# Kernel tuning notes

Measured on AMD Instinct MI355X. Metric: run time of the kernel, lower is better.

The kernel has to match this reference:

```python
import jax, jax.numpy as jnp
import numpy as np

N_NODES = 100000
N_FEAT = 128
HIDDEN = 64
OUT = 16
N_EDGES = 3200000
N_POS = 500000
N_NEG = 500000


def setup_inputs() -> dict:
    key = jax.random.key(0)
    ks = jax.random.split(key, 8)
    x = jax.random.normal(ks[0], (N_NODES, N_FEAT), dtype=jnp.float32)
    edge_index = jax.random.randint(ks[1], (2, N_EDGES), 0, N_NODES, dtype=jnp.int64)
    pos_edge_index = jax.random.randint(ks[2], (2, N_POS), 0, N_NODES, dtype=jnp.int64)
    neg_edge_index = jax.random.randint(ks[3], (2, N_NEG), 0, N_NODES, dtype=jnp.int64)
    W1 = jax.random.normal(ks[4], (N_FEAT, HIDDEN), dtype=jnp.float32) * (1.0 / np.sqrt(N_FEAT))
    b1 = jnp.zeros((HIDDEN,), dtype=jnp.float32)
    W2 = jax.random.normal(ks[5], (HIDDEN, OUT), dtype=jnp.float32) * (1.0 / np.sqrt(HIDDEN))
    b2 = jnp.zeros((OUT,), dtype=jnp.float32)
    return {"x": x, "edge_index": edge_index, "pos_edge_index": pos_edge_index,
            "neg_edge_index": neg_edge_index, "W1": W1, "b1": b1, "W2": W2, "b2": b2}


def gcn_conv(x, W, b, src, dst):
    """PyG GCNConv with add_self_loops=True: D^-1/2 (A+I) D^-1/2 X W + b."""
    n = x.shape[0]
    h = x @ W  # [N, out]
    # degree including self-loop (+1)
    deg = jax.ops.segment_sum(jnp.ones(dst.shape, dtype=h.dtype), dst, num_segments=n) + 1.0
    dis = jax.lax.rsqrt(deg)  # deg >= 1, never inf
    coef = dis[src] * dis[dst]  # [E]
    agg = jax.ops.segment_sum(h[src] * coef[:, None], dst, num_segments=n)
    # self-loop message: norm = dis[i]*dis[i]
    agg = agg + h * (dis * dis)[:, None]
    return agg + b


def reference(x, edge_index, pos_edge_index, neg_edge_index, W1, b1, W2, b2):
    src, dst = edge_index[0], edge_index[1]
    z = jax.nn.relu(gcn_conv(x, W1, b1, src, dst))
    z = gcn_conv(z, W2, b2, src, dst)  # [N, 16]
    ei = jnp.concatenate([pos_edge_index, neg_edge_index], axis=-1)  # [2, P+Q]
    logits = jnp.sum(z[ei[0]] * z[ei[1]], axis=-1)  # [P+Q]
    return logits
```

## Files before the change

kernel.cpp:

```cpp
#include <hip/hip_runtime.h>

#define F 128
#define H 64
#define O 16

#define BSHIFT 7
#define BSZ 128
#define NSUB 8
#define SUBCAP 768
#define ACHUNK 8192
#define XS 136

typedef _Float16 half8_t __attribute__((ext_vector_type(8)));
typedef _Float16 half4_t __attribute__((ext_vector_type(4)));
typedef float f32x4 __attribute__((ext_vector_type(4)));

__global__ void k_bcur2(int* __restrict__ bcur, int NC) {
    int i = blockIdx.x * blockDim.x + threadIdx.x;
    if (i < NC) bcur[i] = i * SUBCAP;
}

__global__ __launch_bounds__(512) void k_bucketA(const int* __restrict__ src,
                                                 const int* __restrict__ dstv,
                                                 int* __restrict__ bcur,
                                                 int* __restrict__ bdata, int E) {
    __shared__ int hist[1024];
    for (int t = threadIdx.x; t < 1024; t += 512) hist[t] = 0;
    __syncthreads();
    int base = blockIdx.x * ACHUNK;
    int end = min(base + ACHUNK, E);
    for (int i = base + threadIdx.x; i < end; i += 512) {
        atomicAdd(&hist[dstv[i] >> BSHIFT], 1);
    }
    __syncthreads();
    int sub = blockIdx.x & (NSUB - 1);
    for (int b = threadIdx.x; b < 1024; b += 512) {
        int c = hist[b];
        if (c > 0) hist[b] = atomicAdd(&bcur[b * NSUB + sub], c);
    }
    __syncthreads();
    for (int i = base + threadIdx.x; i < end; i += 512) {
        int d = dstv[i];
        int b = d >> BSHIFT;
        int pos = atomicAdd(&hist[b], 1);
        bdata[pos] = (src[i] << BSHIFT) | (d & (BSZ - 1));
    }
}

__global__ __launch_bounds__(256) void k_bdeg(const int* __restrict__ bdata,
                                              const int* __restrict__ bcur,
                                              int* __restrict__ deg, int N) {
    __shared__ int h[BSZ];
    int b = blockIdx.x;
    int node0 = b << BSHIFT;
    int nloc = min(BSZ, N - node0);
    for (int t = threadIdx.x; t < BSZ; t += 256) h[t] = 0;
    __syncthreads();
    for (int s = 0; s < NSUB; s++) {
        int start = (b * NSUB + s) * SUBCAP;
        int end = bcur[b * NSUB + s];
        for (int p = start + threadIdx.x; p < end; p += 256)
            atomicAdd(&h[bdata[p] & (BSZ - 1)], 1);
    }
    __syncthreads();
    for (int t = threadIdx.x; t < nloc; t += 256) deg[node0 + t] = h[t];
}

__global__ void k_dis(const int* __restrict__ deg, float* __restrict__ dis, int N) {
    int i = blockIdx.x * blockDim.x + threadIdx.x;
    if (i < N) dis[i] = rsqrtf((float)deg[i] + 1.0f);
}

__global__ void k_scan1(const int* __restrict__ deg, int* __restrict__ local,
                        int* __restrict__ partials, int N) {
    __shared__ int s[256];
    int tid = threadIdx.x;
    int i = blockIdx.x * 256 + tid;
    int v = (i < N) ? deg[i] : 0;
    s[tid] = v;
    __syncthreads();
    for (int off = 1; off < 256; off <<= 1) {
        int t = (tid >= off) ? s[tid - off] : 0;
        __syncthreads();
        s[tid] += t;
        __syncthreads();
    }
    if (i < N) local[i] = s[tid] - v;
    if (tid == 255) partials[blockIdx.x] = s[255];
}

__global__ void k_scan2(int* __restrict__ partials, int NB) {
    __shared__ int s[1024];
    int tid = threadIdx.x;
    int v = (tid < NB) ? partials[tid] : 0;
    s[tid] = v;
    __syncthreads();
    for (int off = 1; off < 1024; off <<= 1) {
        int t = (tid >= off) ? s[tid - off] : 0;
        __syncthreads();
        s[tid] += t;
        __syncthreads();
    }
    partials[tid] = s[tid] - v;
}

__global__ void k_scan3(int* __restrict__ row_ptr, const int* __restrict__ partials,
                        int N, int E) {
    int i = blockIdx.x * blockDim.x + threadIdx.x;
    if (i < N) {
        row_ptr[i] += partials[i >> 8];
    } else if (i == N) {
        row_ptr[N] = E;
    }
}

__global__ __launch_bounds__(256) void k_bplace(const int* __restrict__ bdata,
                                                const int* __restrict__ bcur,
                                                const int* __restrict__ row_ptr,
                                                int* __restrict__ col, int N) {
    __shared__ int cur[BSZ];
    int b = blockIdx.x;
    int node0 = b << BSHIFT;
    int nloc = min(BSZ, N - node0);
    for (int t = threadIdx.x; t < nloc; t += 256) cur[t] = row_ptr[node0 + t];
    __syncthreads();
    for (int s = 0; s < NSUB; s++) {
        int start = (b * NSUB + s) * SUBCAP;
        int end = bcur[b * NSUB + s];
        for (int p = start + threadIdx.x; p < end; p += 256) {
            int v = bdata[p];
            int pos = atomicAdd(&cur[v & (BSZ - 1)], 1);
            col[pos] = v >> BSHIFT;
        }
    }
}

__global__ void k_wprep(const float* __restrict__ W1, _Float16* __restrict__ wt_hi,
                        _Float16* __restrict__ wt_lo) {
    int idx = blockIdx.x * 256 + threadIdx.x;
    int c = idx >> 7, k = idx & 127;
    float w = W1[k * H + c];
    _Float16 hi = (_Float16)w;
    wt_hi[idx] = hi;
    wt_lo[idx] = (_Float16)(w - (float)hi);
}

__global__ __launch_bounds__(256) void k_gemm1(const float* __restrict__ x,
                                               const _Float16* __restrict__ wt_hi,
                                               const _Float16* __restrict__ wt_lo,
                                               const float* __restrict__ dis,
                                               _Float16* __restrict__ h1p, int N) {
    __shared__ _Float16 xh[64 * XS], xl[64 * XS], wh[64 * XS], wl[64 * XS];
    int tid = threadIdx.x;
    int row0 = blockIdx.x * 64;
#pragma unroll
    for (int i = 0; i < 8; i++) {
        int idx = i * 256 + tid;
        int r = idx >> 5;
        int c = (idx & 31) * 4;
        int rr = row0 + r; if (rr >= N) rr = N - 1;
        float4 v = *(const float4*)(x + (size_t)rr * F + c);
        half4_t h = {(_Float16)v.x, (_Float16)v.y, (_Float16)v.z, (_Float16)v.w};
        half4_t l = {(_Float16)(v.x - (float)h[0]), (_Float16)(v.y - (float)h[1]),
                     (_Float16)(v.z - (float)h[2]), (_Float16)(v.w - (float)h[3])};
        *(half4_t*)(xh + r * XS + c) = h;
        *(half4_t*)(xl + r * XS + c) = l;
    }
#pragma unroll
    for (int i = 0; i < 4; i++) {
        int idx = i * 256 + tid;
        int c = idx >> 4;
        int k8 = (idx & 15) * 8;
        *(half8_t*)(wh + c * XS + k8) = *(const half8_t*)(wt_hi + c * 128 + k8);
        *(half8_t*)(wl + c * XS + k8) = *(const half8_t*)(wt_lo + c * 128 + k8);
    }
    __syncthreads();
    int wv = tid >> 6, lane = tid & 63;
    int m = lane & 15, qd = lane >> 4;
    const _Float16* xhp = xh + (wv * 16 + m) * XS;
    const _Float16* xlp = xl + (wv * 16 + m) * XS;
    f32x4 acc[4] = {f32x4{0,0,0,0}, f32x4{0,0,0,0}, f32x4{0,0,0,0}, f32x4{0,0,0,0}};
#pragma unroll
    for (int kc = 0; kc < 4; kc++) {
        int ko = kc * 32 + qd * 8;
        half8_t ah = *(const half8_t*)(xhp + ko);
        half8_t al = *(const half8_t*)(xlp + ko);
#pragma unroll
        for (int nt = 0; nt < 4; nt++) {
            half8_t bh = *(const half8_t*)(wh + (nt * 16 + m) * XS + ko);
            half8_t bl = *(const half8_t*)(wl + (nt * 16 + m) * XS + ko);
            acc[nt] = __builtin_amdgcn_mfma_f32_16x16x32_f16(ah, bh, acc[nt], 0, 0, 0);
            acc[nt] = __builtin_amdgcn_mfma_f32_16x16x32_f16(ah, bl, acc[nt], 0, 0, 0);
            acc[nt] = __builtin_amdgcn_mfma_f32_16x16x32_f16(al, bh, acc[nt], 0, 0, 0);
        }
    }
#pragma unroll
    for (int reg = 0; reg < 4; reg++) {
        int row = row0 + wv * 16 + qd * 4 + reg;
        if (row < N) {
            float d = dis[row];
#pragma unroll
            for (int nt = 0; nt < 4; nt++) {
                h1p[(size_t)row * H + nt * 16 + m] = (_Float16)(acc[nt][reg] * d);
            }
        }
    }
}

__global__ __launch_bounds__(256) void k_gather1(const _Float16* __restrict__ h1p,
                                                 const float* __restrict__ dis,
                                                 const int* __restrict__ row_ptr,
                                                 const int* __restrict__ col,
                                                 const float* __restrict__ b1,
                                                 float* __restrict__ z, int N) {
    int node = blockIdx.x * 4 + (threadIdx.x >> 6);
    if (node >= N) return;
    int lane = threadIdx.x & 63;
    int g = lane >> 3;
    int t = lane & 7;
    const half8_t* hp = (const half8_t*)h1p;
    float acc[8];
#pragma unroll
    for (int j = 0; j < 8; j++) acc[j] = 0.f;
    int e = row_ptr[node + 1];
    for (int p = row_ptr[node] + g; p < e; p += 8) {
        int s = col[p];
        half8_t v = hp[(size_t)s * 8 + t];
#pragma unroll
        for (int j = 0; j < 8; j++) acc[j] += (float)v[j];
    }
#pragma unroll
    for (int off = 8; off < 64; off <<= 1) {
#pragma unroll
        for (int j = 0; j < 8; j++) acc[j] += __shfl_xor(acc[j], off);
    }
    if (g == 0) {
        float dn = dis[node];
        half8_t self = hp[(size_t)node * 8 + t];
        float o[8];
#pragma unroll
        for (int j = 0; j < 8; j++)
            o[j] = fmaxf(fmaf(acc[j] + (float)self[j], dn, b1[t * 8 + j]), 0.f);
        float4* zp = (float4*)(z + (size_t)node * H + t * 8);
        zp[0] = float4{o[0], o[1], o[2], o[3]};
        zp[1] = float4{o[4], o[5], o[6], o[7]};
    }
}

__global__ __launch_bounds__(64) void k_gemm2(const float* __restrict__ z,
                                              const float* __restrict__ W2,
                                              const float* __restrict__ dis,
                                              _Float16* __restrict__ h2p, int N) {
    __shared__ float zs[64 * 65];
    int lane = threadIdx.x;
    int row0 = blockIdx.x * 64;
#pragma unroll
    for (int i = 0; i < 16; i++) {
        int r = i * 4 + (lane >> 4);
        int c = (lane & 15) * 4;
        int rr = row0 + r; if (rr >= N) rr = N - 1;
        float4 v = *(const float4*)(z + (size_t)rr * H + c);
        zs[r * 65 + c + 0] = v.x;
        zs[r * 65 + c + 1] = v.y;
        zs[r * 65 + c + 2] = v.z;
        zs[r * 65 + c + 3] = v.w;
    }
    __syncthreads();
    float acc[O];
#pragma unroll
    for (int c = 0; c < O; c++) acc[c] = 0.f;
#pragma unroll 4
    for (int k = 0; k < H; k++) {
        float a = zs[lane * 65 + k];
        const float* wrow = W2 + (size_t)k * O;
#pragma unroll
        for (int c = 0; c < O; c++) acc[c] = fmaf(a, wrow[c], acc[c]);
    }
    int row = row0 + lane;
    if (row < N) {
        float d = dis[row];
        half8_t* orow = (half8_t*)(h2p + (size_t)row * O);
#pragma unroll
        for (int c0 = 0; c0 < O; c0 += 8) {
            half8_t o;
#pragma unroll
            for (int j = 0; j < 8; j++) o[j] = (_Float16)(acc[c0 + j] * d);
            orow[c0 / 8] = o;
        }
    }
}

__global__ __launch_bounds__(256) void k_gather2(const _Float16* __restrict__ h2p,
                                                 const float* __restrict__ dis,
                                                 const int* __restrict__ row_ptr,
                                                 const int* __restrict__ col,
                                                 const float* __restrict__ b2,
                                                 float* __restrict__ z2, int N) {
    int node = blockIdx.x * 4 + (threadIdx.x >> 6);
    if (node >= N) return;
    int lane = threadIdx.x & 63;
    int g = lane >> 1;
    int t = lane & 1;
    const half8_t* hp = (const half8_t*)h2p;
    float acc[8];
#pragma unroll
    for (int j = 0; j < 8; j++) acc[j] = 0.f;
    int e = row_ptr[node + 1];
    for (int p = row_ptr[node] + g; p < e; p += 32) {
        int s = col[p];
        half8_t v = hp[(size_t)s * 2 + t];
#pragma unroll
        for (int j = 0; j < 8; j++) acc[j] += (float)v[j];
    }
#pragma unroll
    for (int off = 2; off < 64; off <<= 1) {
#pragma unroll
        for (int j = 0; j < 8; j++) acc[j] += __shfl_xor(acc[j], off);
    }
    if (g == 0) {
        float dn = dis[node];
        half8_t self = hp[(size_t)node * 2 + t];
        float o[8];
#pragma unroll
        for (int j = 0; j < 8; j++)
            o[j] = fmaf(acc[j] + (float)self[j], dn, b2[t * 8 + j]);
        float4* zp = (float4*)(z2 + (size_t)node * O + t * 8);
        zp[0] = float4{o[0], o[1], o[2], o[3]};
        zp[1] = float4{o[4], o[5], o[6], o[7]};
    }
}

__global__ __launch_bounds__(256) void k_logits(const float* __restrict__ z2,
                                                const int* __restrict__ pos,
                                                const int* __restrict__ neg,
                                                float* __restrict__ out, int P, int Q) {
    int tid = blockIdx.x * 256 + threadIdx.x;
    int i = tid >> 2;
    if (i >= P + Q) return;
    int k = tid & 3;
    int a, b;
    if (i < P) { a = pos[i]; b = pos[P + i]; }
    else       { int t = i - P; a = neg[t]; b = neg[Q + t]; }
    float4 va = *(const float4*)(z2 + (size_t)a * O + k * 4);
    float4 vb = *(const float4*)(z2 + (size_t)b * O + k * 4);
    float r = va.x * vb.x + va.y * vb.y + va.z * vb.z + va.w * vb.w;
    r += __shfl_xor(r, 1);
    r += __shfl_xor(r, 2);
    if (k == 0) out[i] = r;
}

extern "C" void kernel_launch(void* const* d_in, const int* in_sizes, int n_in,
                              void* d_out, int out_size, void* d_ws, size_t ws_size,
                              hipStream_t stream) {
    const float* x   = (const float*)d_in[0];
    const int*   ei  = (const int*)d_in[1];
    const int*   pos = (const int*)d_in[2];
    const int*   neg = (const int*)d_in[3];
    const float* W1  = (const float*)d_in[4];
    const float* b1  = (const float*)d_in[5];
    const float* W2  = (const float*)d_in[6];
    const float* b2  = (const float*)d_in[7];
    float* out = (float*)d_out;

    int N = in_sizes[0] / F;
    int E = in_sizes[1] / 2;
    int P = in_sizes[2] / 2;
    int Q = in_sizes[3] / 2;
    const int* src  = ei;
    const int* dstv = ei + E;

    int NB  = (N + 255) / 256;
    int Npad = NB * 256;
    int Epad = (E + 63) & ~63;
    int NBK = (N + BSZ - 1) / BSZ;
    int NC  = NBK * NSUB;

    char* w = (char*)d_ws;
    int*   deg      = (int*)w;        w += (size_t)Npad * 4;
    float* dis      = (float*)w;      w += (size_t)Npad * 4;
    int*   row_ptr  = (int*)w;        w += (size_t)(Npad + 256) * 4;
    int*   bcur     = (int*)w;        w += 8192 * 4;
    int*   partials = (int*)w;        w += 1024 * 4;
    int*   col      = (int*)w;        w += (size_t)Epad * 4;
    _Float16* h1p   = (_Float16*)w;
    int*      bdata = (int*)w;
    size_t h1b = (size_t)N * H * 2, bdb = (size_t)NC * SUBCAP * 4;
    w += (h1b > bdb ? h1b : bdb);
    float*    z     = (float*)w;      w += (size_t)N * H * 4;
    _Float16* h2p   = (_Float16*)w;   w += (size_t)N * O * 2;
    float*    z2    = (float*)w;      w += (size_t)N * O * 4;
    _Float16* wt_hi = (_Float16*)w;   w += (size_t)H * F * 2;
    _Float16* wt_lo = (_Float16*)w;

    k_wprep<<<(H * F + 255) / 256, 256, 0, stream>>>(W1, wt_hi, wt_lo);

    k_bcur2<<<(NC + 255) / 256, 256, 0, stream>>>(bcur, NC);
    k_bucketA<<<(E + ACHUNK - 1) / ACHUNK, 512, 0, stream>>>(src, dstv, bcur, bdata, E);
    k_bdeg<<<NBK, 256, 0, stream>>>(bdata, bcur, deg, N);
    k_dis<<<(N + 255) / 256, 256, 0, stream>>>(deg, dis, N);
    k_scan1<<<NB, 256, 0, stream>>>(deg, row_ptr, partials, N);
    k_scan2<<<1, 1024, 0, stream>>>(partials, NB);
    k_scan3<<<(N + 256) / 256, 256, 0, stream>>>(row_ptr, partials, N, E);
    k_bplace<<<NBK, 256, 0, stream>>>(bdata, bcur, row_ptr, col, N);

    k_gemm1<<<(N + 63) / 64, 256, 0, stream>>>(x, wt_hi, wt_lo, dis, h1p, N);
    k_gather1<<<(N + 3) / 4, 256, 0, stream>>>(h1p, dis, row_ptr, col, b1, z, N);

    k_gemm2<<<(N + 63) / 64, 64, 0, stream>>>(z, W2, dis, h2p, N);
    k_gather2<<<(N + 3) / 4, 256, 0, stream>>>(h2p, dis, row_ptr, col, b2, z2, N);

    k_logits<<<((P + Q) * 4 + 255) / 256, 256, 0, stream>>>(z2, pos, neg, out, P, Q);
}
```

Before: 345.2 us.

## Fuse degree scan into bucket pipeline and unroll gather1 edge loop

Folds the rsqrt degree normalization into the bucket degree kernel. It replaces the three-kernel global prefix scan with a per-bucket scan over bucket counts plus an in-block scan inside the placement kernel, which also writes row_ptr. This drops three kernel launches and one pass over the degree array. The gather1 edge loop is also unrolled by two so that more independent loads are in flight.

```diff
diff --git a/kernel.cpp b/kernel.cpp
--- a/kernel.cpp
+++ b/kernel.cpp
@@ -49,7 +49,8 @@
 
 __global__ __launch_bounds__(256) void k_bdeg(const int* __restrict__ bdata,
                                               const int* __restrict__ bcur,
-                                              int* __restrict__ deg, int N) {
+                                              int* __restrict__ deg,
+                                              float* __restrict__ dis, int N) {
     __shared__ int h[BSZ];
     int b = blockIdx.x;
     int node0 = b << BSHIFT;
@@ -63,71 +64,68 @@
             atomicAdd(&h[bdata[p] & (BSZ - 1)], 1);
     }
     __syncthreads();
-    for (int t = threadIdx.x; t < nloc; t += 256) deg[node0 + t] = h[t];
-}
-
-__global__ void k_dis(const int* __restrict__ deg, float* __restrict__ dis, int N) {
-    int i = blockIdx.x * blockDim.x + threadIdx.x;
-    if (i < N) dis[i] = rsqrtf((float)deg[i] + 1.0f);
-}
-
-__global__ void k_scan1(const int* __restrict__ deg, int* __restrict__ local,
-                        int* __restrict__ partials, int N) {
-    __shared__ int s[256];
-    int tid = threadIdx.x;
-    int i = blockIdx.x * 256 + tid;
-    int v = (i < N) ? deg[i] : 0;
-    s[tid] = v;
-    __syncthreads();
-    for (int off = 1; off < 256; off <<= 1) {
-        int t = (tid >= off) ? s[tid - off] : 0;
-        __syncthreads();
-        s[tid] += t;
-        __syncthreads();
-    }
-    if (i < N) local[i] = s[tid] - v;
-    if (tid == 255) partials[blockIdx.x] = s[255];
-}
-
-__global__ void k_scan2(int* __restrict__ partials, int NB) {
+    for (int t = threadIdx.x; t < nloc; t += 256) {
+        int d = h[t];
+        deg[node0 + t] = d;
+        dis[node0 + t] = rsqrtf((float)d + 1.0f);
+    }
+}
+
+__global__ void k_bscan(const int* __restrict__ bcur, int* __restrict__ bstart, int NBK) {
     __shared__ int s[1024];
     int tid = threadIdx.x;
-    int v = (tid < NB) ? partials[tid] : 0;
-    s[tid] = v;
+    int tot = 0;
+    if (tid < NBK) {
+        for (int ss = 0; ss < NSUB; ss++)
+            tot += bcur[tid * NSUB + ss] - (tid * NSUB + ss) * SUBCAP;
+    }
+    s[tid] = tot;
     __syncthreads();
     for (int off = 1; off < 1024; off <<= 1) {
-        int t = (tid >= off) ? s[tid - off] : 0;
+        int v = (tid >= off) ? s[tid - off] : 0;
         __syncthreads();
-        s[tid] += t;
+        s[tid] += v;
         __syncthreads();
     }
-    partials[tid] = s[tid] - v;
-}
-
-__global__ void k_scan3(int* __restrict__ row_ptr, const int* __restrict__ partials,
-                        int N, int E) {
-    int i = blockIdx.x * blockDim.x + threadIdx.x;
-    if (i < N) {
-        row_ptr[i] += partials[i >> 8];
-    } else if (i == N) {
-        row_ptr[N] = E;
-    }
+    bstart[tid] = s[tid] - tot;
 }
 
 __global__ __launch_bounds__(256) void k_bplace(const int* __restrict__ bdata,
                                                 const int* __restrict__ bcur,
-                                                const int* __restrict__ row_ptr,
+                                                const int* __restrict__ deg,
+                                                const int* __restrict__ bstart,
+                                                int* __restrict__ row_ptr,
                                                 int* __restrict__ col, int N) {
+    __shared__ int pref[BSZ];
     __shared__ int cur[BSZ];
     int b = blockIdx.x;
     int node0 = b << BSHIFT;
     int nloc = min(BSZ, N - node0);
-    for (int t = threadIdx.x; t < nloc; t += 256) cur[t] = row_ptr[node0 + t];
+    int tid = threadIdx.x;
+    int myDeg = 0;
+    if (tid < BSZ) {
+        myDeg = (tid < nloc) ? deg[node0 + tid] : 0;
+        pref[tid] = myDeg;
+    }
+    __syncthreads();
+    for (int off = 1; off < BSZ; off <<= 1) {
+        int v = (tid < BSZ && tid >= off) ? pref[tid - off] : 0;
+        __syncthreads();
+        if (tid < BSZ) pref[tid] += v;
+        __syncthreads();
+    }
+    int base = bstart[b];
+    if (tid < nloc) {
+        int excl = base + pref[tid] - myDeg;
+        cur[tid] = excl;
+        row_ptr[node0 + tid] = excl;
+    }
+    if (tid == 0) row_ptr[node0 + nloc] = base + pref[BSZ - 1];
     __syncthreads();
     for (int s = 0; s < NSUB; s++) {
         int start = (b * NSUB + s) * SUBCAP;
         int end = bcur[b * NSUB + s];
-        for (int p = start + threadIdx.x; p < end; p += 256) {
+        for (int p = start + tid; p < end; p += 256) {
             int v = bdata[p];
             int pos = atomicAdd(&cur[v & (BSZ - 1)], 1);
             col[pos] = v >> BSHIFT;
@@ -223,11 +221,21 @@
 #pragma unroll
     for (int j = 0; j < 8; j++) acc[j] = 0.f;
     int e = row_ptr[node + 1];
-    for (int p = row_ptr[node] + g; p < e; p += 8) {
-        int s = col[p];
-        half8_t v = hp[(size_t)s * 8 + t];
-#pragma unroll
-        for (int j = 0; j < 8; j++) acc[j] += (float)v[j];
+    int p = row_ptr[node] + g;
+    for (; p + 8 < e; p += 16) {
+        int s0 = col[p], s1 = col[p + 8];
+        half8_t v0 = hp[(size_t)s0 * 8 + t];
+        half8_t v1 = hp[(size_t)s1 * 8 + t];
+#pragma unroll
+        for (int j = 0; j < 8; j++) acc[j] += (float)v0[j];
+#pragma unroll
+        for (int j = 0; j < 8; j++) acc[j] += (float)v1[j];
+    }
+    if (p < e) {
+        int s0 = col[p];
+        half8_t v0 = hp[(size_t)s0 * 8 + t];
+#pragma unroll
+        for (int j = 0; j < 8; j++) acc[j] += (float)v0[j];
     }
 #pragma unroll
     for (int off = 8; off < 64; off <<= 1) {
@@ -369,19 +377,18 @@
     const int* src  = ei;
     const int* dstv = ei + E;
 
-    int NB  = (N + 255) / 256;
-    int Npad = NB * 256;
+    int Npad = ((N + 255) / 256) * 256;
     int Epad = (E + 63) & ~63;
     int NBK = (N + BSZ - 1) / BSZ;
     int NC  = NBK * NSUB;
 
     char* w = (char*)d_ws;
-    int*   deg      = (int*)w;        w += (size_t)Npad * 4;
-    float* dis      = (float*)w;      w += (size_t)Npad * 4;
-    int*   row_ptr  = (int*)w;        w += (size_t)(Npad + 256) * 4;
-    int*   bcur     = (int*)w;        w += 8192 * 4;
-    int*   partials = (int*)w;        w += 1024 * 4;
-    int*   col      = (int*)w;        w += (size_t)Epad * 4;
+    int*      deg   = (int*)w;        w += (size_t)Npad * 4;
+    float*    dis   = (float*)w;      w += (size_t)Npad * 4;
+    int*      row_ptr = (int*)w;      w += (size_t)(Npad + 256) * 4;
+    int*      bcur  = (int*)w;        w += 8192 * 4;
+    int*      bstart = (int*)w;       w += 1024 * 4;
+    int*      col   = (int*)w;        w += (size_t)Epad * 4;
     _Float16* h1p   = (_Float16*)w;
     int*      bdata = (int*)w;
     size_t h1b = (size_t)N * H * 2, bdb = (size_t)NC * SUBCAP * 4;
@@ -393,15 +400,11 @@
     _Float16* wt_lo = (_Float16*)w;
 
     k_wprep<<<(H * F + 255) / 256, 256, 0, stream>>>(W1, wt_hi, wt_lo);
-
     k_bcur2<<<(NC + 255) / 256, 256, 0, stream>>>(bcur, NC);
     k_bucketA<<<(E + ACHUNK - 1) / ACHUNK, 512, 0, stream>>>(src, dstv, bcur, bdata, E);
-    k_bdeg<<<NBK, 256, 0, stream>>>(bdata, bcur, deg, N);
-    k_dis<<<(N + 255) / 256, 256, 0, stream>>>(deg, dis, N);
-    k_scan1<<<NB, 256, 0, stream>>>(deg, row_ptr, partials, N);
-    k_scan2<<<1, 1024, 0, stream>>>(partials, NB);
-    k_scan3<<<(N + 256) / 256, 256, 0, stream>>>(row_ptr, partials, N, E);
-    k_bplace<<<NBK, 256, 0, stream>>>(bdata, bcur, row_ptr, col, N);
+    k_bdeg<<<NBK, 256, 0, stream>>>(bdata, bcur, deg, dis, N);
+    k_bscan<<<1, 1024, 0, stream>>>(bcur, bstart, NBK);
+    k_bplace<<<NBK, 256, 0, stream>>>(bdata, bcur, deg, bstart, row_ptr, col, N);
 
     k_gemm1<<<(N + 63) / 64, 256, 0, stream>>>(x, wt_hi, wt_lo, dis, h1p, N);
     k_gather1<<<(N + 3) / 4, 256, 0, stream>>>(h1p, dis, row_ptr, col, b1, z, N);
```

Measured after the change: 330.5 us. 1.04x faster.
